# Kernel tuning notes

Hardware: AMD Instinct MI355X
Metric: run time of the kernel (lower is better)

## Reference

```python
import jax, jax.numpy as jnp
import numpy as np

H = 16
D_MODEL = 1024
D_K = D_MODEL // H
NEG = -1e9


def setup_inputs() -> dict:
    key = jax.random.key(0)
    ks = jax.random.split(key, 12)
    B, S = 2, 2048
    inp = {
        "query": jax.random.normal(ks[0], (B, S, D_MODEL), jnp.float32),
        "key": jax.random.normal(ks[1], (B, S, D_MODEL), jnp.float32),
        "value": jax.random.normal(ks[2], (B, S, D_MODEL), jnp.float32),
        "mask": jnp.ones((B, 1, S), jnp.int32),
    }
    s = 1.0 / np.sqrt(D_MODEL)
    for i, nm in enumerate(["Wq", "Wk", "Wv", "Wo"]):
        inp[nm] = jax.random.normal(ks[3 + i], (D_MODEL, D_MODEL), jnp.float32) * s
        inp["b" + nm[1]] = jax.random.normal(ks[7 + i], (D_MODEL,), jnp.float32) * s
    return inp


def _split_heads(x):
    B, S, _ = x.shape
    return x.reshape(B, S, H, D_K).transpose(0, 2, 1, 3)  # [B,H,S,Dk]


def reference(query, key, value, mask, Wq, bq, Wk, bk, Wv, bv, Wo, bo):
    q = _split_heads(query @ Wq + bq)
    k = _split_heads(key @ Wk + bk)
    v = _split_heads(value @ Wv + bv)
    scores = jnp.einsum("bhqd,bhkd->bhqk", q, k) / jnp.sqrt(jnp.float32(D_K))
    # mask [B,1,Sk] -> broadcast as [B,1,1,Sk]
    scores = jnp.where(mask[:, None, :, :] == 0, NEG, scores)
    attn = jax.nn.softmax(scores, axis=-1)  # dropout is identity in eval mode
    out = jnp.einsum("bhqk,bhkd->bhqd", attn, v)
    B, _, Sq, _ = out.shape
    out = out.transpose(0, 2, 1, 3).reshape(B, Sq, H * D_K)
    return out @ Wo + bo
```

## Files before the change

### kernel.cpp

```cpp
#include <hip/hip_runtime.h>
#include <hip/hip_bf16.h>

typedef __attribute__((ext_vector_type(8))) short short8;
typedef __attribute__((ext_vector_type(4))) float float4v;
typedef __hip_bfloat16 bf16;

#define MFMA16(a, b, c) __builtin_amdgcn_mfma_f32_16x16x32_bf16((a), (b), (c), 0, 0, 0)

static __device__ __forceinline__ short8 load8(const bf16* p) {
    return *reinterpret_cast<const short8*>(p);
}
static __device__ __forceinline__ unsigned short bfu(float x) {
    union { bf16 b; unsigned short u; } c; c.b = __float2bfloat16(x); return c.u;
}
static __device__ __forceinline__ unsigned pack2(float lo, float hi) {
    return ((unsigned)bfu(hi) << 16) | bfu(lo);
}
static __device__ __forceinline__ short bf_bits(float x) {
    union { bf16 b; short u; } c; c.b = __float2bfloat16(x); return c.u;
}
static __device__ __forceinline__ short8 cvt8(float4 a, float4 b) {
    short8 r;
    r[0] = bf_bits(a.x); r[1] = bf_bits(a.y); r[2] = bf_bits(a.z); r[3] = bf_bits(a.w);
    r[4] = bf_bits(b.x); r[5] = bf_bits(b.y); r[6] = bf_bits(b.z); r[7] = bf_bits(b.w);
    return r;
}

typedef const __attribute__((address_space(1))) unsigned int* gp1;
typedef __attribute__((address_space(3))) unsigned int* lp3;
static __device__ __forceinline__ void async16(const void* g, void* l) {
    __builtin_amdgcn_global_load_lds((gp1)g, (lp3)l, 16, 0, 0);
}

__global__ __launch_bounds__(256) void transpose_w(
    const float* __restrict__ in, bf16* __restrict__ out)
{
    __shared__ bf16 tile[64][65];
    int tx = threadIdx.x, ty = threadIdx.y;
    int bx = blockIdx.x * 64, by = blockIdx.y * 64;
    for (int i = ty; i < 64; i += 4)
        tile[i][tx] = __float2bfloat16(in[(size_t)(by + i) * 1024 + bx + tx]);
    __syncthreads();
    for (int i = ty; i < 64; i += 4)
        out[(size_t)(bx + i) * 1024 + by + tx] = tile[tx][i];
}

__global__ __launch_bounds__(256, 3) void qkv_gemm(
    const float* __restrict__ Xq, const float* __restrict__ Xk,
    const float* __restrict__ Xv, const bf16* __restrict__ Wt_all,
    const float* __restrict__ bq, const float* __restrict__ bk,
    const float* __restrict__ bv,
    bf16* __restrict__ outq, bf16* __restrict__ outk, bf16* __restrict__ outv)
{
    __shared__ float As[128 * 32];
    __shared__ bf16  Bs[128 * 32];

    int z = blockIdx.z;
    const float* X    = (z == 0) ? Xq : (z == 1) ? Xk : Xv;
    const float* bias = (z == 0) ? bq : (z == 1) ? bk : bv;
    const bf16*  Wt   = Wt_all + (size_t)z * 1048576;
    bf16*        out  = (z == 0) ? outq : (z == 1) ? outk : outv;
    bool vmode = (z == 2);

    int tid = threadIdx.x;
    int w = tid >> 6, lane = tid & 63, l16 = lane & 15, quad = lane >> 4;
    int m_base = blockIdx.y * 128, n_base = blockIdx.x * 128;

    int ra = lane >> 3;
    int sa = (lane & 7) ^ (ra & 7);
    int rb = lane >> 2;
    int sb = (lane & 3) ^ (rb & 3);
    const float* Asrc = X  + (size_t)(m_base + w * 8 + ra) * 1024 + sa * 4;
    const bf16*  Bsrc = Wt + (size_t)(n_base + w * 16 + rb) * 1024 + sb * 8;
    char* Adst = (char*)As + w * 1024;
    char* Bdst = (char*)Bs + w * 1024;

    int wm = (w & 1) * 64, wn = (w >> 1) * 64;

    float4v zero = {0.f, 0.f, 0.f, 0.f};
    float4v acc[4][4];
    #pragma unroll
    for (int mi = 0; mi < 4; ++mi)
        #pragma unroll
        for (int nj = 0; nj < 4; ++nj) acc[mi][nj] = zero;

    for (int kt = 0; kt < 1024; kt += 32) {
        #pragma unroll
        for (int p = 0; p < 4; ++p)
            async16(Asrc + (size_t)p * 32 * 1024 + kt, Adst + p * 4096);
        #pragma unroll
        for (int p = 0; p < 2; ++p)
            async16(Bsrc + (size_t)p * 64 * 1024 + kt, Bdst + p * 4096);
        __syncthreads();

        short8 af[4], bf[4];
        #pragma unroll
        for (int mi = 0; mi < 4; ++mi) {
            const float* rp = As + (wm + mi * 16 + l16) * 32;
            float4 f0 = *(const float4*)(rp + (((quad * 2)     ^ (l16 & 7)) << 2));
            float4 f1 = *(const float4*)(rp + (((quad * 2 + 1) ^ (l16 & 7)) << 2));
            af[mi] = cvt8(f0, f1);
        }
        #pragma unroll
        for (int nj = 0; nj < 4; ++nj) {
            const bf16* rp = Bs + (wn + nj * 16 + l16) * 32;
            bf[nj] = load8(rp + ((quad ^ (l16 & 3)) << 3));
        }
        #pragma unroll
        for (int mi = 0; mi < 4; ++mi)
            #pragma unroll
            for (int nj = 0; nj < 4; ++nj)
                acc[mi][nj] = MFMA16(af[mi], bf[nj], acc[mi][nj]);
        __syncthreads();
    }

    float bsv[4];
    #pragma unroll
    for (int nj = 0; nj < 4; ++nj)
        bsv[nj] = bias[n_base + wn + nj * 16 + l16];

    #pragma unroll
    for (int mi = 0; mi < 4; ++mi) {
        #pragma unroll
        for (int nj = 0; nj < 4; ++nj) {
            int n = n_base + wn + nj * 16 + l16;
            int h = n >> 6, dk = n & 63;
            int m0 = m_base + wm + mi * 16 + quad * 4;
            int b = m0 >> 11, s0 = m0 & 2047;
            if (vmode) {
                float v0 = acc[mi][nj][0] + bsv[nj];
                float v1 = acc[mi][nj][1] + bsv[nj];
                float v2 = acc[mi][nj][2] + bsv[nj];
                float v3 = acc[mi][nj][3] + bsv[nj];
                uint2 pv; pv.x = pack2(v0, v1); pv.y = pack2(v2, v3);
                size_t idx = ((size_t)(b * 16 + h) * 64 + dk) * 2048 + s0;
                *reinterpret_cast<uint2*>(out + idx) = pv;
            } else {
                #pragma unroll
                for (int r = 0; r < 4; ++r) {
                    size_t idx = (((size_t)(b * 16 + h) * 2048 + s0 + r) * 64 + dk);
                    out[idx] = __float2bfloat16(acc[mi][nj][r] + bsv[nj]);
                }
            }
        }
    }
}

__global__ __launch_bounds__(256, 3) void out_gemm(
    const bf16* __restrict__ A, const bf16* __restrict__ Wt,
    const float* __restrict__ bias, float* __restrict__ out)
{
    __shared__ bf16 As[128 * 32];
    __shared__ bf16 Bs[128 * 32];

    int tid = threadIdx.x;
    int w = tid >> 6, lane = tid & 63, l16 = lane & 15, quad = lane >> 4;
    int m_base = blockIdx.y * 128, n_base = blockIdx.x * 128;

    int rr = lane >> 2;
    int ss = (lane & 3) ^ (rr & 3);
    const bf16* Asrc = A  + (size_t)(m_base + w * 16 + rr) * 1024 + ss * 8;
    const bf16* Bsrc = Wt + (size_t)(n_base + w * 16 + rr) * 1024 + ss * 8;
    char* Adst = (char*)As + w * 1024;
    char* Bdst = (char*)Bs + w * 1024;

    int wm = (w & 1) * 64, wn = (w >> 1) * 64;

    float4v zero = {0.f, 0.f, 0.f, 0.f};
    float4v acc[4][4];
    #pragma unroll
    for (int mi = 0; mi < 4; ++mi)
        #pragma unroll
        for (int nj = 0; nj < 4; ++nj) acc[mi][nj] = zero;

    for (int kt = 0; kt < 1024; kt += 32) {
        #pragma unroll
        for (int p = 0; p < 2; ++p) {
            async16(Asrc + (size_t)p * 64 * 1024 + kt, Adst + p * 4096);
            async16(Bsrc + (size_t)p * 64 * 1024 + kt, Bdst + p * 4096);
        }
        __syncthreads();

        short8 af[4], bf[4];
        #pragma unroll
        for (int mi = 0; mi < 4; ++mi) {
            const bf16* rp = As + (wm + mi * 16 + l16) * 32;
            af[mi] = load8(rp + ((quad ^ (l16 & 3)) << 3));
        }
        #pragma unroll
        for (int nj = 0; nj < 4; ++nj) {
            const bf16* rp = Bs + (wn + nj * 16 + l16) * 32;
            bf[nj] = load8(rp + ((quad ^ (l16 & 3)) << 3));
        }
        #pragma unroll
        for (int mi = 0; mi < 4; ++mi)
            #pragma unroll
            for (int nj = 0; nj < 4; ++nj)
                acc[mi][nj] = MFMA16(af[mi], bf[nj], acc[mi][nj]);
        __syncthreads();
    }

    float bsv[4];
    #pragma unroll
    for (int nj = 0; nj < 4; ++nj)
        bsv[nj] = bias[n_base + wn + nj * 16 + l16];

    #pragma unroll
    for (int mi = 0; mi < 4; ++mi)
        #pragma unroll
        for (int nj = 0; nj < 4; ++nj) {
            int n = n_base + wn + nj * 16 + l16;
            int m0 = m_base + wm + mi * 16 + quad * 4;
            #pragma unroll
            for (int r = 0; r < 4; ++r)
                out[(size_t)(m0 + r) * 1024 + n] = acc[mi][nj][r] + bsv[nj];
        }
}

__global__ __launch_bounds__(256, 2) void attn_fused(
    const bf16* __restrict__ Qm, const bf16* __restrict__ Km,
    const bf16* __restrict__ Vt, const int* __restrict__ mask,
    bf16* __restrict__ Oout)
{
    __shared__ float biasL[2048];
    __shared__ __align__(16) bf16 Kc[64 * 64];
    __shared__ __align__(16) bf16 Vc[64 * 64];
    __shared__ __align__(16) bf16 P[4][32 * 72];

    int tid = threadIdx.x;
    int w = tid >> 6, lane = tid & 63, l16 = lane & 15, quad = lane >> 4;
    int bh = blockIdx.x >> 4, qg = blockIdx.x & 15;
    int b = bh >> 4, h = bh & 15;
    int tile0 = (qg * 4 + w) * 2;

    const int* mb = mask + b * 2048;
    for (int i = tid; i < 2048; i += 256)
        biasL[i] = (mb[i] == 0) ? -2.0e9f : 0.0f;

    short8 bQ[2][2];
    #pragma unroll
    for (int qi = 0; qi < 2; ++qi) {
        const bf16* Qb = Qm + ((size_t)bh * 2048 + (size_t)(tile0 + qi) * 16) * 64;
        bQ[qi][0] = load8(Qb + l16 * 64 + quad * 8);
        bQ[qi][1] = load8(Qb + l16 * 64 + 32 + quad * 8);
    }

    int r8 = lane >> 3;
    int sl = (lane & 7) ^ (r8 & 7);
    const bf16* Kb = Km + (size_t)bh * 2048 * 64;
    const bf16* Vb = Vt + (size_t)bh * 64 * 2048;
    const bf16* Ksrc = Kb + (size_t)(w * 8 + r8) * 64 + sl * 8;
    const bf16* Vsrc = Vb + (size_t)(w * 8 + r8) * 2048 + sl * 8;
    char* Kdst = (char*)Kc + w * 1024;
    char* Vdst = (char*)Vc + w * 1024;

    bf16* Pw = &P[w][0];
    int sw = l16 & 7;

    float4v zero = {0.f, 0.f, 0.f, 0.f};
    float4v Oacc[2][4];
    #pragma unroll
    for (int qi = 0; qi < 2; ++qi)
        #pragma unroll
        for (int g = 0; g < 4; ++g) Oacc[qi][g] = zero;
    float lsum[2] = {0.f, 0.f};
    const float C = 0.18033688f;

    for (int kt = 0; kt < 2048; kt += 64) {
        async16(Ksrc + (size_t)kt * 64, Kdst);
        async16(Ksrc + (size_t)(kt + 32) * 64, Kdst + 4096);
        async16(Vsrc + kt, Vdst);
        async16(Vsrc + (size_t)32 * 2048 + kt, Vdst + 4096);
        __syncthreads();

        float4v S[2][4];
        #pragma unroll
        for (int kj = 0; kj < 4; ++kj) {
            const bf16* kr = Kc + (kj * 16 + l16) * 64;
            short8 a0 = load8(kr + (((0 + quad) ^ sw) << 3));
            short8 a1 = load8(kr + (((4 + quad) ^ sw) << 3));
            #pragma unroll
            for (int qi = 0; qi < 2; ++qi) {
                float4v s = zero;
                s = MFMA16(a0, bQ[qi][0], s);
                s = MFMA16(a1, bQ[qi][1], s);
                S[qi][kj] = s;
            }
        }

        #pragma unroll
        for (int kj = 0; kj < 4; ++kj) {
            float4 bv4 = *reinterpret_cast<const float4*>(&biasL[kt + kj * 16 + quad * 4]);
            const float* bb = reinterpret_cast<const float*>(&bv4);
            #pragma unroll
            for (int qi = 0; qi < 2; ++qi) {
                float p[4];
                #pragma unroll
                for (int r = 0; r < 4; ++r)
                    p[r] = __builtin_amdgcn_exp2f(
                        fminf(fmaf(S[qi][kj][r], C, bb[r]), 80.f));
                lsum[qi] += (p[0] + p[1]) + (p[2] + p[3]);
                uint2 pw; pw.x = pack2(p[0], p[1]); pw.y = pack2(p[2], p[3]);
                *reinterpret_cast<uint2*>(
                    &Pw[(qi * 16 + l16) * 72 + kj * 16 + quad * 4]) = pw;
            }
        }

        short8 ap[2][2];
        #pragma unroll
        for (int qi = 0; qi < 2; ++qi) {
            ap[qi][0] = load8(&Pw[(qi * 16 + l16) * 72 + quad * 8]);
            ap[qi][1] = load8(&Pw[(qi * 16 + l16) * 72 + 32 + quad * 8]);
        }
        #pragma unroll
        for (int g = 0; g < 4; ++g) {
            const bf16* vr = Vc + (g * 16 + l16) * 64;
            short8 v0 = load8(vr + (((0 + quad) ^ sw) << 3));
            short8 v1 = load8(vr + (((4 + quad) ^ sw) << 3));
            #pragma unroll
            for (int qi = 0; qi < 2; ++qi) {
                Oacc[qi][g] = MFMA16(ap[qi][0], v0, Oacc[qi][g]);
                Oacc[qi][g] = MFMA16(ap[qi][1], v1, Oacc[qi][g]);
            }
        }
        __syncthreads();
    }

    #pragma unroll
    for (int qi = 0; qi < 2; ++qi) {
        float ls = lsum[qi];
        ls += __shfl_xor(ls, 16, 64);
        ls += __shfl_xor(ls, 32, 64);
        #pragma unroll
        for (int r = 0; r < 4; ++r) {
            float linv = 1.f / __shfl(ls, quad * 4 + r, 64);
            int srow = (tile0 + qi) * 16 + quad * 4 + r;
            size_t base = ((size_t)b * 2048 + srow) * 1024 + h * 64;
            #pragma unroll
            for (int g = 0; g < 4; ++g)
                Oout[base + g * 16 + l16] = __float2bfloat16(Oacc[qi][g][r] * linv);
        }
    }
}

extern "C" void kernel_launch(void* const* d_in, const int* in_sizes, int n_in,
                              void* d_out, int out_size, void* d_ws, size_t ws_size,
                              hipStream_t stream) {
    const float* query = (const float*)d_in[0];
    const float* key   = (const float*)d_in[1];
    const float* value = (const float*)d_in[2];
    const int*   mask  = (const int*)d_in[3];
    const float* Wq = (const float*)d_in[4];
    const float* bq = (const float*)d_in[5];
    const float* Wk = (const float*)d_in[6];
    const float* bk = (const float*)d_in[7];
    const float* Wv = (const float*)d_in[8];
    const float* bv = (const float*)d_in[9];
    const float* Wo = (const float*)d_in[10];
    const float* bo = (const float*)d_in[11];

    char* ws = (char*)d_ws;
    const size_t MB = 1024 * 1024;
    bf16* vb     = (bf16*)ws;
    bf16* Wt_all = (bf16*)(ws + 8 * MB);
    bf16* aout   = (bf16*)(ws + 8 * MB);
    bf16* WtO    = (bf16*)ws;
    bf16* qb     = (bf16*)d_out;
    bf16* kb     = (bf16*)((char*)d_out + 8 * MB);
    float* out   = (float*)d_out;

    dim3 tgrid(16, 16), tblk(64, 4);

    transpose_w<<<tgrid, tblk, 0, stream>>>(Wq, Wt_all);
    transpose_w<<<tgrid, tblk, 0, stream>>>(Wk, Wt_all + 1048576);
    transpose_w<<<tgrid, tblk, 0, stream>>>(Wv, Wt_all + 2097152);

    qkv_gemm<<<dim3(8, 32, 3), 256, 0, stream>>>(
        query, key, value, Wt_all, bq, bk, bv, qb, kb, vb);

    attn_fused<<<dim3(512), dim3(256), 0, stream>>>(qb, kb, vb, mask, aout);

    transpose_w<<<tgrid, tblk, 0, stream>>>(Wo, WtO);
    out_gemm<<<dim3(8, 32), 256, 0, stream>>>(aout, WtO, bo, out);
}
```

Measured before the change: 280.8 us.

## Double-buffer LDS tiles in GEMM and attention kernels, merge QKV transposes

Adds a two-stage LDS double buffer to the QKV GEMM, the output GEMM and the fused attention kernel, so the async global-to-LDS loads for the next tile run while the current tile is computed, with one barrier per iteration. The three weight transposes for Q, K and V become a single launch with a z grid dimension. The output GEMM moves to 128x64 tiles with a launch bound of 2, which doubles the grid. The softmax exponent clamp is removed to save an instruction. The cost is more LDS per block and lower occupancy. Dropping the clamp also risks overflow when logits are large, since no running max is subtracted.

```diff
diff --git a/kernel.cpp b/kernel.cpp
--- a/kernel.cpp
+++ b/kernel.cpp
@@ -32,7 +32,23 @@
     __builtin_amdgcn_global_load_lds((gp1)g, (lp3)l, 16, 0, 0);
 }
 
-__global__ __launch_bounds__(256) void transpose_w(
+__global__ __launch_bounds__(256) void transpose_qkv(
+    const float* __restrict__ Wq, const float* __restrict__ Wk,
+    const float* __restrict__ Wv, bf16* __restrict__ out_base)
+{
+    __shared__ bf16 tile[64][65];
+    const float* in = (blockIdx.z == 0) ? Wq : (blockIdx.z == 1) ? Wk : Wv;
+    bf16* out = out_base + (size_t)blockIdx.z * 1048576;
+    int tx = threadIdx.x, ty = threadIdx.y;
+    int bx = blockIdx.x * 64, by = blockIdx.y * 64;
+    for (int i = ty; i < 64; i += 4)
+        tile[i][tx] = __float2bfloat16(in[(size_t)(by + i) * 1024 + bx + tx]);
+    __syncthreads();
+    for (int i = ty; i < 64; i += 4)
+        out[(size_t)(bx + i) * 1024 + by + tx] = tile[tx][i];
+}
+
+__global__ __launch_bounds__(256) void transpose_one(
     const float* __restrict__ in, bf16* __restrict__ out)
 {
     __shared__ bf16 tile[64][65];
@@ -52,8 +68,8 @@
     const float* __restrict__ bv,
     bf16* __restrict__ outq, bf16* __restrict__ outk, bf16* __restrict__ outv)
 {
-    __shared__ float As[128 * 32];
-    __shared__ bf16  Bs[128 * 32];
+    __shared__ float As[2][128 * 32];
+    __shared__ bf16  Bs[2][128 * 32];
 
     int z = blockIdx.z;
     const float* X    = (z == 0) ? Xq : (z == 1) ? Xk : Xv;
@@ -72,8 +88,6 @@
     int sb = (lane & 3) ^ (rb & 3);
     const float* Asrc = X  + (size_t)(m_base + w * 8 + ra) * 1024 + sa * 4;
     const bf16*  Bsrc = Wt + (size_t)(n_base + w * 16 + rb) * 1024 + sb * 8;
-    char* Adst = (char*)As + w * 1024;
-    char* Bdst = (char*)Bs + w * 1024;
 
     int wm = (w & 1) * 64, wn = (w >> 1) * 64;
 
@@ -84,26 +98,38 @@
         #pragma unroll
         for (int nj = 0; nj < 4; ++nj) acc[mi][nj] = zero;
 
-    for (int kt = 0; kt < 1024; kt += 32) {
+    #pragma unroll
+    for (int p = 0; p < 4; ++p)
+        async16(Asrc + (size_t)p * 32 * 1024, (char*)As[0] + w * 1024 + p * 4096);
+    #pragma unroll
+    for (int p = 0; p < 2; ++p)
+        async16(Bsrc + (size_t)p * 64 * 1024, (char*)Bs[0] + w * 1024 + p * 4096);
+    __syncthreads();
+
+    for (int it = 0; it < 32; ++it) {
+        int cur = it & 1, nxt = cur ^ 1;
+        int kn = ((it + 1) & 31) * 32;
+
         #pragma unroll
         for (int p = 0; p < 4; ++p)
-            async16(Asrc + (size_t)p * 32 * 1024 + kt, Adst + p * 4096);
+            async16(Asrc + (size_t)p * 32 * 1024 + kn,
+                    (char*)As[nxt] + w * 1024 + p * 4096);
         #pragma unroll
         for (int p = 0; p < 2; ++p)
-            async16(Bsrc + (size_t)p * 64 * 1024 + kt, Bdst + p * 4096);
-        __syncthreads();
+            async16(Bsrc + (size_t)p * 64 * 1024 + kn,
+                    (char*)Bs[nxt] + w * 1024 + p * 4096);
 
         short8 af[4], bf[4];
         #pragma unroll
         for (int mi = 0; mi < 4; ++mi) {
-            const float* rp = As + (wm + mi * 16 + l16) * 32;
+            const float* rp = As[cur] + (wm + mi * 16 + l16) * 32;
             float4 f0 = *(const float4*)(rp + (((quad * 2)     ^ (l16 & 7)) << 2));
             float4 f1 = *(const float4*)(rp + (((quad * 2 + 1) ^ (l16 & 7)) << 2));
             af[mi] = cvt8(f0, f1);
         }
         #pragma unroll
         for (int nj = 0; nj < 4; ++nj) {
-            const bf16* rp = Bs + (wn + nj * 16 + l16) * 32;
+            const bf16* rp = Bs[cur] + (wn + nj * 16 + l16) * 32;
             bf[nj] = load8(rp + ((quad ^ (l16 & 3)) << 3));
         }
         #pragma unroll
@@ -146,69 +172,75 @@
     }
 }
 
-__global__ __launch_bounds__(256, 3) void out_gemm(
+__global__ __launch_bounds__(256, 2) void out_gemm(
     const bf16* __restrict__ A, const bf16* __restrict__ Wt,
     const float* __restrict__ bias, float* __restrict__ out)
 {
-    __shared__ bf16 As[128 * 32];
-    __shared__ bf16 Bs[128 * 32];
+    __shared__ bf16 As[2][128 * 32];
+    __shared__ bf16 Bs[2][64 * 32];
 
     int tid = threadIdx.x;
     int w = tid >> 6, lane = tid & 63, l16 = lane & 15, quad = lane >> 4;
-    int m_base = blockIdx.y * 128, n_base = blockIdx.x * 128;
+    int m_base = blockIdx.y * 128, n_base = blockIdx.x * 64;
 
     int rr = lane >> 2;
     int ss = (lane & 3) ^ (rr & 3);
     const bf16* Asrc = A  + (size_t)(m_base + w * 16 + rr) * 1024 + ss * 8;
     const bf16* Bsrc = Wt + (size_t)(n_base + w * 16 + rr) * 1024 + ss * 8;
-    char* Adst = (char*)As + w * 1024;
-    char* Bdst = (char*)Bs + w * 1024;
-
-    int wm = (w & 1) * 64, wn = (w >> 1) * 64;
+
+    int wm = (w & 1) * 64, wn = (w >> 1) * 32;
 
     float4v zero = {0.f, 0.f, 0.f, 0.f};
-    float4v acc[4][4];
+    float4v acc[4][2];
     #pragma unroll
     for (int mi = 0; mi < 4; ++mi)
         #pragma unroll
-        for (int nj = 0; nj < 4; ++nj) acc[mi][nj] = zero;
-
-    for (int kt = 0; kt < 1024; kt += 32) {
-        #pragma unroll
-        for (int p = 0; p < 2; ++p) {
-            async16(Asrc + (size_t)p * 64 * 1024 + kt, Adst + p * 4096);
-            async16(Bsrc + (size_t)p * 64 * 1024 + kt, Bdst + p * 4096);
-        }
-        __syncthreads();
-
-        short8 af[4], bf[4];
+        for (int nj = 0; nj < 2; ++nj) acc[mi][nj] = zero;
+
+    #pragma unroll
+    for (int p = 0; p < 2; ++p)
+        async16(Asrc + (size_t)p * 64 * 1024, (char*)As[0] + w * 1024 + p * 4096);
+    async16(Bsrc, (char*)Bs[0] + w * 1024);
+    __syncthreads();
+
+    for (int it = 0; it < 32; ++it) {
+        int cur = it & 1, nxt = cur ^ 1;
+        int kn = ((it + 1) & 31) * 32;
+
+        #pragma unroll
+        for (int p = 0; p < 2; ++p)
+            async16(Asrc + (size_t)p * 64 * 1024 + kn,
+                    (char*)As[nxt] + w * 1024 + p * 4096);
+        async16(Bsrc + kn, (char*)Bs[nxt] + w * 1024);
+
+        short8 af[4], bf[2];
         #pragma unroll
         for (int mi = 0; mi < 4; ++mi) {
-            const bf16* rp = As + (wm + mi * 16 + l16) * 32;
+            const bf16* rp = As[cur] + (wm + mi * 16 + l16) * 32;
             af[mi] = load8(rp + ((quad ^ (l16 & 3)) << 3));
         }
         #pragma unroll
-        for (int nj = 0; nj < 4; ++nj) {
-            const bf16* rp = Bs + (wn + nj * 16 + l16) * 32;
+        for (int nj = 0; nj < 2; ++nj) {
+            const bf16* rp = Bs[cur] + (wn + nj * 16 + l16) * 32;
             bf[nj] = load8(rp + ((quad ^ (l16 & 3)) << 3));
         }
         #pragma unroll
         for (int mi = 0; mi < 4; ++mi)
             #pragma unroll
-            for (int nj = 0; nj < 4; ++nj)
+            for (int nj = 0; nj < 2; ++nj)
                 acc[mi][nj] = MFMA16(af[mi], bf[nj], acc[mi][nj]);
         __syncthreads();
     }
 
-    float bsv[4];
-    #pragma unroll
-    for (int nj = 0; nj < 4; ++nj)
+    float bsv[2];
+    #pragma unroll
+    for (int nj = 0; nj < 2; ++nj)
         bsv[nj] = bias[n_base + wn + nj * 16 + l16];
 
     #pragma unroll
     for (int mi = 0; mi < 4; ++mi)
         #pragma unroll
-        for (int nj = 0; nj < 4; ++nj) {
+        for (int nj = 0; nj < 2; ++nj) {
             int n = n_base + wn + nj * 16 + l16;
             int m0 = m_base + wm + mi * 16 + quad * 4;
             #pragma unroll
@@ -223,8 +255,8 @@
     bf16* __restrict__ Oout)
 {
     __shared__ float biasL[2048];
-    __shared__ __align__(16) bf16 Kc[64 * 64];
-    __shared__ __align__(16) bf16 Vc[64 * 64];
+    __shared__ __align__(16) bf16 Kc[2][64 * 64];
+    __shared__ __align__(16) bf16 Vc[2][64 * 64];
     __shared__ __align__(16) bf16 P[4][32 * 72];
 
     int tid = threadIdx.x;
@@ -251,8 +283,6 @@
     const bf16* Vb = Vt + (size_t)bh * 64 * 2048;
     const bf16* Ksrc = Kb + (size_t)(w * 8 + r8) * 64 + sl * 8;
     const bf16* Vsrc = Vb + (size_t)(w * 8 + r8) * 2048 + sl * 8;
-    char* Kdst = (char*)Kc + w * 1024;
-    char* Vdst = (char*)Vc + w * 1024;
 
     bf16* Pw = &P[w][0];
     int sw = l16 & 7;
@@ -266,17 +296,26 @@
     float lsum[2] = {0.f, 0.f};
     const float C = 0.18033688f;
 
-    for (int kt = 0; kt < 2048; kt += 64) {
-        async16(Ksrc + (size_t)kt * 64, Kdst);
-        async16(Ksrc + (size_t)(kt + 32) * 64, Kdst + 4096);
-        async16(Vsrc + kt, Vdst);
-        async16(Vsrc + (size_t)32 * 2048 + kt, Vdst + 4096);
-        __syncthreads();
+    async16(Ksrc, (char*)Kc[0] + w * 1024);
+    async16(Ksrc + (size_t)32 * 64, (char*)Kc[0] + w * 1024 + 4096);
+    async16(Vsrc, (char*)Vc[0] + w * 1024);
+    async16(Vsrc + (size_t)32 * 2048, (char*)Vc[0] + w * 1024 + 4096);
+    __syncthreads();
+
+    for (int it = 0; it < 32; ++it) {
+        int cur = it & 1, nxt = cur ^ 1;
+        int kt = it * 64;
+        int kn = ((it + 1) & 31) * 64;
+
+        async16(Ksrc + (size_t)kn * 64, (char*)Kc[nxt] + w * 1024);
+        async16(Ksrc + (size_t)(kn + 32) * 64, (char*)Kc[nxt] + w * 1024 + 4096);
+        async16(Vsrc + kn, (char*)Vc[nxt] + w * 1024);
+        async16(Vsrc + (size_t)32 * 2048 + kn, (char*)Vc[nxt] + w * 1024 + 4096);
 
         float4v S[2][4];
         #pragma unroll
         for (int kj = 0; kj < 4; ++kj) {
-            const bf16* kr = Kc + (kj * 16 + l16) * 64;
+            const bf16* kr = Kc[cur] + (kj * 16 + l16) * 64;
             short8 a0 = load8(kr + (((0 + quad) ^ sw) << 3));
             short8 a1 = load8(kr + (((4 + quad) ^ sw) << 3));
             #pragma unroll
@@ -297,8 +336,7 @@
                 float p[4];
                 #pragma unroll
                 for (int r = 0; r < 4; ++r)
-                    p[r] = __builtin_amdgcn_exp2f(
-                        fminf(fmaf(S[qi][kj][r], C, bb[r]), 80.f));
+                    p[r] = __builtin_amdgcn_exp2f(fmaf(S[qi][kj][r], C, bb[r]));
                 lsum[qi] += (p[0] + p[1]) + (p[2] + p[3]);
                 uint2 pw; pw.x = pack2(p[0], p[1]); pw.y = pack2(p[2], p[3]);
                 *reinterpret_cast<uint2*>(
@@ -314,7 +352,7 @@
         }
         #pragma unroll
         for (int g = 0; g < 4; ++g) {
-            const bf16* vr = Vc + (g * 16 + l16) * 64;
+            const bf16* vr = Vc[cur] + (g * 16 + l16) * 64;
             short8 v0 = load8(vr + (((0 + quad) ^ sw) << 3));
             short8 v1 = load8(vr + (((4 + quad) ^ sw) << 3));
             #pragma unroll
@@ -369,17 +407,14 @@
     bf16* kb     = (bf16*)((char*)d_out + 8 * MB);
     float* out   = (float*)d_out;
 
-    dim3 tgrid(16, 16), tblk(64, 4);
-
-    transpose_w<<<tgrid, tblk, 0, stream>>>(Wq, Wt_all);
-    transpose_w<<<tgrid, tblk, 0, stream>>>(Wk, Wt_all + 1048576);
-    transpose_w<<<tgrid, tblk, 0, stream>>>(Wv, Wt_all + 2097152);
+    transpose_qkv<<<dim3(16, 16, 3), dim3(64, 4), 0, stream>>>(Wq, Wk, Wv, Wt_all);
 
     qkv_gemm<<<dim3(8, 32, 3), 256, 0, stream>>>(
         query, key, value, Wt_all, bq, bk, bv, qb, kb, vb);
 
     attn_fused<<<dim3(512), dim3(256), 0, stream>>>(qb, kb, vb, mask, aout);
 
-    transpose_w<<<tgrid, tblk, 0, stream>>>(Wo, WtO);
-    out_gemm<<<dim3(8, 32), 256, 0, stream>>>(aout, WtO, bo, out);
-}
+    transpose_one<<<dim3(16, 16), dim3(64, 4), 0, stream>>>(Wo, WtO);
+
+    out_gemm<<<dim3(16, 32), 256, 0, stream>>>(aout, WtO, bo, out);
+}
```

Result: faster. 271.2 us (-3.4%).
